# Performance work log

Hardware: AMD Instinct MI355X
Metric: run time of the kernel (lower is better)

The kernel has to match this reference:

```python
import jax, jax.numpy as jnp
import numpy as np

B, T, S, PD = 512, 2048, 16, 4

def setup_inputs() -> dict:
    key = jax.random.key(0)
    ks = jax.random.split(key, 10)
    w = lambda k, sh: (jax.random.normal(k, sh, dtype=jnp.float32) * 0.1)
    return {
        'z': jax.random.normal(ks[0], (B, T, S), dtype=jnp.float32),
        'p': jax.random.normal(ks[1], (B, T, PD), dtype=jnp.float32),
        'mu0': jnp.zeros((B, S), dtype=jnp.float32),
        'P0': jnp.full((B, S), 0.1, dtype=jnp.float32),  # cfg['kf_P0']
        'Wq1': w(ks[2], (PD, 64)), 'bq1': jnp.zeros((64,), jnp.float32),
        'Wq2': w(ks[3], (64, S)),  'bq2': jnp.zeros((S,), jnp.float32),
        'Wr1': w(ks[4], (PD, 64)), 'br1': jnp.zeros((64,), jnp.float32),
        'Wr2': w(ks[5], (64, S)),  'br2': jnp.zeros((S,), jnp.float32),
        'Wg1': w(ks[6], (PD, 32)), 'bg1': jnp.zeros((32,), jnp.float32),
        'Wg2': w(ks[7], (32, 1)),  'bg2': jnp.zeros((1,), jnp.float32),
    }

def _mlp(x, W1, b1, W2, b2):
    return jax.nn.relu(x @ W1 + b1) @ W2 + b2

def reference(z, p, mu0, P0, Wq1, bq1, Wq2, bq2, Wr1, br1, Wr2, br2, Wg1, bg1, Wg2, bg2):
    # z: [B,T,S], p: [B,T,PD]; scan over time with batched Kalman state.
    zT = jnp.swapaxes(z, 0, 1)  # [T,B,S]
    pT = jnp.swapaxes(p, 0, 1)  # [T,B,PD]

    def step(carry, inp):
        mu, P = carry            # [B,S], [B,S]
        z_t, p_t = inp           # [B,S], [B,PD]
        Q_t = jax.nn.softplus(_mlp(p_t, Wq1, bq1, Wq2, bq2)) + 1e-8
        R_t = jax.nn.softplus(_mlp(p_t, Wr1, br1, Wr2, br2)) + 1e-8
        P_pred = P + Q_t
        K = jnp.clip(P_pred / (P_pred + R_t), 1e-6, 0.95)
        gamma_t = jax.nn.sigmoid(_mlp(p_t, Wg1, bg1, Wg2, bg2))  # [B,1] (scalar per sample)
        mu_new = mu + gamma_t * (K * (z_t - mu))
        P_new = (1.0 - K) * P_pred
        return (mu_new, P_new), mu_new

    (mu_f, P_f), mus = jax.lax.scan(step, (mu0, P0), (zT, pT))
    return jnp.swapaxes(mus, 0, 1)  # [B,T,S]
```

## Files before the change

kernel.cpp:

```cpp
#include <hip/hip_runtime.h>
#include <hip/hip_fp16.h>
#include <stdint.h>
#include <math.h>

#define KB 512
#define KT 2048
#define KS 16
#define KPD 4

typedef _Float16 f16;
typedef _Float16 f16x4v __attribute__((ext_vector_type(4)));
typedef _Float16 f16x8 __attribute__((ext_vector_type(8)));
typedef float f32x4 __attribute__((ext_vector_type(4)));

#define MFMA16(A, B, C) __builtin_amdgcn_mfma_f32_16x16x32_f16(A, B, C, 0, 0, 0)

__device__ __forceinline__ float softplus_f(float x) {
    float ax = fabsf(x);
    float e  = __expf(-ax);
    return fmaxf(x, 0.0f) + __logf(1.0f + e);
}
__device__ __forceinline__ float sigmoid_f(float x) {
    return __builtin_amdgcn_rcpf(1.0f + __expf(-x));
}
__device__ __forceinline__ float h2f_lo(uint32_t w) {
    return __half2float(__ushort_as_half((unsigned short)(w & 0xffffu)));
}
__device__ __forceinline__ float h2f_hi(uint32_t w) {
    return __half2float(__ushort_as_half((unsigned short)(w >> 16)));
}
__device__ __forceinline__ f16x8 zero8() {
    f16x8 v;
#pragma unroll
    for (int i = 0; i < 8; ++i) v[i] = (f16)0;
    return v;
}

#define HRS 168

__global__ __launch_bounds__(64) void mlp_kernel(
    const float* __restrict__ p,
    const float* __restrict__ Wq1, const float* __restrict__ bq1,
    const float* __restrict__ Wq2, const float* __restrict__ bq2,
    const float* __restrict__ Wr1, const float* __restrict__ br1,
    const float* __restrict__ Wr2, const float* __restrict__ br2,
    const float* __restrict__ Wg1, const float* __restrict__ bg1,
    const float* __restrict__ Wg2, const float* __restrict__ bg2,
    uint32_t* __restrict__ qr_ws, float* __restrict__ g_ws)
{
    __shared__ __align__(16) f16 Hl[64][HRS];
    __shared__ __align__(16) f16 Pl[64][4];

    const int l = threadIdx.x;
    const int g = l >> 4;
    const int c = l & 15;
    const int row0 = blockIdx.x * 64;
    const int b = row0 >> 11;
    const int t0 = row0 & (KT - 1);

    f16x8 fA1[10];
#pragma unroll
    for (int m = 0; m < 10; ++m) {
        const float* W = (m < 4) ? (Wq1 + m * 16)
                       : (m < 8) ? (Wr1 + (m - 4) * 16)
                                 : (Wg1 + (m - 8) * 16);
        const int ld = (m < 8) ? 64 : 32;
        float w0 = W[0 * ld + c], w1 = W[1 * ld + c],
              w2 = W[2 * ld + c], w3 = W[3 * ld + c];
        f16x8 a = zero8();
        if (g == 0) { a[0] = (f16)w0; a[1] = (f16)w1; a[2] = (f16)w2; a[3] = (f16)w3; }
        fA1[m] = a;
    }

    f16x8 fA2[5];
#pragma unroll
    for (int i = 0; i < 4; ++i) {
        const float* W = (i < 2) ? Wq2 : Wr2;
        const int kb = (i & 1) * 32;
        f16x8 a;
#pragma unroll
        for (int j = 0; j < 8; ++j) a[j] = (f16)W[(kb + g * 8 + j) * 16 + c];
        fA2[i] = a;
    }
    {
        f16x8 a = zero8();
        if (c == 0) {
#pragma unroll
            for (int j = 0; j < 8; ++j) a[j] = (f16)Wg2[g * 8 + j];
        }
        fA2[4] = a;
    }

    const float bQ0 = bq2[g * 4 + 0], bQ1 = bq2[g * 4 + 1],
                bQ2 = bq2[g * 4 + 2], bQ3 = bq2[g * 4 + 3];
    const float bR0 = br2[g * 4 + 0], bR1 = br2[g * 4 + 1],
                bR2 = br2[g * 4 + 2], bR3 = br2[g * 4 + 3];
    const float bG = bg2[0];

    {
        const float4 pv = *reinterpret_cast<const float4*>(p + (size_t)(row0 + l) * KPD);
        f16x4v v; v[0] = (f16)pv.x; v[1] = (f16)pv.y; v[2] = (f16)pv.z; v[3] = (f16)pv.w;
        *reinterpret_cast<f16x4v*>(&Pl[l][0]) = v;
    }
    asm volatile("s_waitcnt lgkmcnt(0)" ::: "memory");
    __builtin_amdgcn_sched_barrier(0);

    f16x8 fBP[4];
#pragma unroll
    for (int n = 0; n < 4; ++n) {
        f16x8 v = zero8();
        if (g == 0) {
            f16x4v q = *reinterpret_cast<const f16x4v*>(&Pl[n * 16 + c][0]);
            v[0] = q[0]; v[1] = q[1]; v[2] = q[2]; v[3] = q[3];
        }
        fBP[n] = v;
    }

#pragma unroll
    for (int m = 0; m < 10; ++m) {
        const float* bs = (m < 4) ? (bq1 + m * 16)
                        : (m < 8) ? (br1 + (m - 4) * 16)
                                  : (bg1 + (m - 8) * 16);
        const float b0 = bs[g * 4 + 0], b1 = bs[g * 4 + 1],
                    b2 = bs[g * 4 + 2], b3 = bs[g * 4 + 3];
#pragma unroll
        for (int n = 0; n < 4; ++n) {
            f32x4 acc; acc[0] = b0; acc[1] = b1; acc[2] = b2; acc[3] = b3;
            acc = MFMA16(fA1[m], fBP[n], acc);
            auto h01 = __builtin_amdgcn_cvt_pkrtz(fmaxf(acc[0], 0.f), fmaxf(acc[1], 0.f));
            auto h23 = __builtin_amdgcn_cvt_pkrtz(fmaxf(acc[2], 0.f), fmaxf(acc[3], 0.f));
            uint2 w;
            __builtin_memcpy(&w.x, &h01, 4);
            __builtin_memcpy(&w.y, &h23, 4);
            *reinterpret_cast<uint2*>(&Hl[n * 16 + c][m * 16 + g * 4]) = w;
        }
    }
    asm volatile("s_waitcnt lgkmcnt(0)" ::: "memory");
    __builtin_amdgcn_sched_barrier(0);

#pragma unroll
    for (int n = 0; n < 4; ++n) {
        const int bt = n * 16 + c;
        f16x8 fb0 = *reinterpret_cast<const f16x8*>(&Hl[bt][0 * 32 + g * 8]);
        f16x8 fb1 = *reinterpret_cast<const f16x8*>(&Hl[bt][1 * 32 + g * 8]);
        f16x8 fb2 = *reinterpret_cast<const f16x8*>(&Hl[bt][2 * 32 + g * 8]);
        f16x8 fb3 = *reinterpret_cast<const f16x8*>(&Hl[bt][3 * 32 + g * 8]);
        f16x8 fb4 = *reinterpret_cast<const f16x8*>(&Hl[bt][4 * 32 + g * 8]);

        f32x4 aq; aq[0] = bQ0; aq[1] = bQ1; aq[2] = bQ2; aq[3] = bQ3;
        aq = MFMA16(fA2[0], fb0, aq);
        aq = MFMA16(fA2[1], fb1, aq);
        f32x4 ar; ar[0] = bR0; ar[1] = bR1; ar[2] = bR2; ar[3] = bR3;
        ar = MFMA16(fA2[2], fb2, ar);
        ar = MFMA16(fA2[3], fb3, ar);
        f32x4 ag; ag[0] = 0.f; ag[1] = 0.f; ag[2] = 0.f; ag[3] = 0.f;
        ag = MFMA16(fA2[4], fb4, ag);

        uint32_t* qdst = qr_ws + ((size_t)b * KS + g * 4) * KT + t0 + bt;
#pragma unroll
        for (int i = 0; i < 4; ++i) {
            float Qv = softplus_f(aq[i]) + 1e-8f;
            float Rv = softplus_f(ar[i]) + 1e-8f;
            auto pk = __builtin_amdgcn_cvt_pkrtz(Qv, Rv);
            uint32_t w; __builtin_memcpy(&w, &pk, 4);
            qdst[(size_t)i * KT] = w;
        }
        if (g == 0)
            g_ws[(size_t)b * KT + t0 + bt] = sigmoid_f(ag[0] + bG);
    }
}

#define QT 512
#define NQ (KT / QT)
#define CL 8

__global__ __launch_bounds__(1024) void scan_kernel(
    const uint32_t* __restrict__ qr_ws, const float* __restrict__ g_ws,
    const float* __restrict__ z, const float* __restrict__ mu0,
    const float* __restrict__ P0, float* __restrict__ out)
{
    __shared__ float smem[QT * 17 + QT];
    float* zmu = smem;
    float* gl  = smem + QT * 17;

    const int b = blockIdx.x;
    const int tid = threadIdx.x;
    const int lane = tid & 63;
    const int s = tid >> 6;

    const uint32_t* qrow = qr_ws + (size_t)(b * KS + s) * KT;
    const float* zb = z + (size_t)b * KT * KS;
    const float* gb = g_ws + (size_t)b * KT;
    float* ob = out + (size_t)b * KT * KS;

    float P_q  = P0[b * KS + s];
    float mu_q = mu0[b * KS + s];

    for (int q = 0; q < NQ; ++q) {
        const int t0 = q * QT;

        {
            const float4* zq = reinterpret_cast<const float4*>(zb + (size_t)t0 * KS);
#pragma unroll
            for (int v = 0; v < 2; ++v) {
                int k = tid * 2 + v;
                float4 w = zq[k];
                int t = k >> 2, s0 = (k & 3) << 2;
                zmu[t * 17 + s0 + 0] = w.x;
                zmu[t * 17 + s0 + 1] = w.y;
                zmu[t * 17 + s0 + 2] = w.z;
                zmu[t * 17 + s0 + 3] = w.w;
            }
            if (tid < QT) gl[tid] = gb[t0 + tid];
        }
        __syncthreads();

        uint32_t qr[CL];
        {
            const uint4* qp = reinterpret_cast<const uint4*>(qrow + t0 + lane * CL);
            uint4 u0 = qp[0], u1 = qp[1];
            qr[0] = u0.x; qr[1] = u0.y; qr[2] = u0.z; qr[3] = u0.w;
            qr[4] = u1.x; qr[5] = u1.y; qr[6] = u1.z; qr[7] = u1.w;
        }
        float c00 = 1.f, c01 = 0.f, c10 = 0.f, c11 = 1.f;
#pragma unroll
        for (int i = 0; i < CL; ++i) {
            float Q = h2f_lo(qr[i]), R = h2f_hi(qr[i]);
            float ta = fmaf(Q, c10, c00);
            float tb = fmaf(Q, c11, c01);
            float n10 = fmaf(Q + R, c10, c00);
            float n11 = fmaf(Q + R, c11, c01);
            c00 = R * ta; c01 = R * tb; c10 = n10; c11 = n11;
        }
        float rn = __builtin_amdgcn_rcpf(c11);
        float ma = c00 * rn, mb = c01 * rn, mc = c10 * rn;

#pragma unroll
        for (int r = 0; r < 6; ++r) {
            const int d = 1 << r;
            float pa = __shfl_up(ma, d);
            float pb = __shfl_up(mb, d);
            float pc = __shfl_up(mc, d);
            float na = fmaf(ma, pa, mb * pc);
            float nb = fmaf(ma, pb, mb);
            float nc = fmaf(mc, pa, pc);
            float nd = fmaf(mc, pb, 1.f);
            float rr = __builtin_amdgcn_rcpf(nd);
            bool act = (lane >= d);
            ma = act ? na * rr : ma;
            mb = act ? nb * rr : mb;
            mc = act ? nc * rr : mc;
        }
        float ea = __shfl_up(ma, 1);
        float eb = __shfl_up(mb, 1);
        float ec = __shfl_up(mc, 1);
        if (lane == 0) { ea = 1.f; eb = 0.f; ec = 0.f; }
        float P = fmaf(ea, P_q, eb) * __builtin_amdgcn_rcpf(fmaf(ec, P_q, 1.f));

        float av[CL], bw[CL];
        float A = 1.f, Bv = 0.f;
#pragma unroll
        for (int i = 0; i < CL; ++i) {
            float Q = h2f_lo(qr[i]), R = h2f_hi(qr[i]);
            float Pp = P + Q;
            float K0 = Pp * __builtin_amdgcn_rcpf(Pp + R);
            float Kk = __builtin_amdgcn_fmed3f(K0, 1e-6f, 0.95f);
            int t = lane * CL + i;
            float g = gl[t];
            float gk = g * Kk;
            float zv = zmu[t * 17 + s];
            av[i] = 1.f - gk;
            bw[i] = gk * zv;
            P = fmaf(-Kk, Pp, Pp);
            A = A * av[i];
            Bv = fmaf(av[i], Bv, bw[i]);
        }
        float P_end = __shfl(P, 63);

#pragma unroll
        for (int r = 0; r < 6; ++r) {
            const int d = 1 << r;
            float pA = __shfl_up(A, d);
            float pB = __shfl_up(Bv, d);
            float nA = A * pA;
            float nB = fmaf(A, pB, Bv);
            bool act = (lane >= d);
            A  = act ? nA : A;
            Bv = act ? nB : Bv;
        }
        float eA = __shfl_up(A, 1);
        float eB = __shfl_up(Bv, 1);
        if (lane == 0) { eA = 1.f; eB = 0.f; }
        float mu = fmaf(eA, mu_q, eB);

        __syncthreads();

#pragma unroll
        for (int i = 0; i < CL; ++i) {
            mu = fmaf(av[i], mu, bw[i]);
            zmu[(lane * CL + i) * 17 + s] = mu;
        }
        float mu_end = __shfl(mu, 63);
        __syncthreads();

#pragma unroll
        for (int v = 0; v < 2; ++v) {
            int k = tid * 2 + v;
            int t = k >> 2, s0 = (k & 3) << 2;
            float4 w;
            w.x = zmu[t * 17 + s0 + 0];
            w.y = zmu[t * 17 + s0 + 1];
            w.z = zmu[t * 17 + s0 + 2];
            w.w = zmu[t * 17 + s0 + 3];
            *reinterpret_cast<float4*>(ob + (size_t)(t0 + t) * KS + s0) = w;
        }
        P_q  = P_end;
        mu_q = mu_end;
        __syncthreads();
    }
}

#define KTT 128
#define KNT (KT / KTT)
#define SROW (KS + 1)

__device__ __forceinline__ void mlp16(const float4 pv,
    const float* __restrict__ W1, const float* __restrict__ b1,
    const float* __restrict__ W2, const float* __restrict__ b2,
    float* __restrict__ acc)
{
#pragma unroll
    for (int j = 0; j < KS; ++j) acc[j] = b2[j];
#pragma unroll 4
    for (int k = 0; k < 64; ++k) {
        float hk = b1[k];
        hk = fmaf(pv.x, W1[k],       hk);
        hk = fmaf(pv.y, W1[64 + k],  hk);
        hk = fmaf(pv.z, W1[128 + k], hk);
        hk = fmaf(pv.w, W1[192 + k], hk);
        hk = fmaxf(hk, 0.0f);
#pragma unroll
        for (int j = 0; j < KS; ++j) acc[j] = fmaf(hk, W2[k * KS + j], acc[j]);
    }
}

__global__ __launch_bounds__(320, 2) void kalman_fused(
    const float* __restrict__ z, const float* __restrict__ p,
    const float* __restrict__ mu0, const float* __restrict__ P0,
    const float* __restrict__ Wq1, const float* __restrict__ bq1,
    const float* __restrict__ Wq2, const float* __restrict__ bq2,
    const float* __restrict__ Wr1, const float* __restrict__ br1,
    const float* __restrict__ Wr2, const float* __restrict__ br2,
    const float* __restrict__ Wg1, const float* __restrict__ bg1,
    const float* __restrict__ Wg2, const float* __restrict__ bg2,
    float* __restrict__ out)
{
    __shared__ float sQ[2][KTT][SROW];
    __shared__ float sR[2][KTT][SROW];
    __shared__ float sZf[2][KTT][KS];
    __shared__ float sGf[2][KTT];

    const int b = blockIdx.x;
    const int tid = threadIdx.x;
    const float* __restrict__ zb = z + (size_t)b * KT * KS;
    const float* __restrict__ pb = p + (size_t)b * KT * KPD;
    float* __restrict__ outb = out + (size_t)b * KT * KS;

    const bool is_mlp = (tid < 256);

    auto do_mlp_tile = [&](int tile, int buf) {
        const int tt = tid & (KTT - 1);
        const int t = tile * KTT + tt;
        const float4 pv = *reinterpret_cast<const float4*>(pb + (size_t)t * KPD);
        float acc[KS];
        if (tid < KTT) {
            mlp16(pv, Wq1, bq1, Wq2, bq2, acc);
#pragma unroll
            for (int j = 0; j < KS; ++j)
                sQ[buf][tt][j] = softplus_f(acc[j]) + 1e-8f;
            float ag = bg2[0];
#pragma unroll 8
            for (int k = 0; k < 32; ++k) {
                float hk = bg1[k];
                hk = fmaf(pv.x, Wg1[k],      hk);
                hk = fmaf(pv.y, Wg1[32 + k], hk);
                hk = fmaf(pv.z, Wg1[64 + k], hk);
                hk = fmaf(pv.w, Wg1[96 + k], hk);
                hk = fmaxf(hk, 0.0f);
                ag = fmaf(hk, Wg2[k], ag);
            }
            sGf[buf][tt] = sigmoid_f(ag);
        } else {
            mlp16(pv, Wr1, br1, Wr2, br2, acc);
#pragma unroll
            for (int j = 0; j < KS; ++j)
                sR[buf][tt][j] = softplus_f(acc[j]) + 1e-8f;
        }
        const float4* __restrict__ zt =
            reinterpret_cast<const float4*>(zb + (size_t)tile * KTT * KS);
        float4* __restrict__ zd = reinterpret_cast<float4*>(&sZf[buf][0][0]);
        zd[tid] = zt[tid];
        zd[tid + 256] = zt[tid + 256];
    };

    float mu = 0.0f, Pv = 0.0f;
    if (!is_mlp) {
        const int lane = tid - 256;
        if (lane < KS) {
            mu = mu0[(size_t)b * KS + lane];
            Pv = P0[(size_t)b * KS + lane];
        }
    }

    if (is_mlp) do_mlp_tile(0, 0);
    __syncthreads();

    for (int k = 0; k < KNT; ++k) {
        const int cur = k & 1;
        if (is_mlp) {
            if (k + 1 < KNT) do_mlp_tile(k + 1, cur ^ 1);
        } else {
            const int lane = tid - 256;
            if (lane < KS) {
                const int s = lane;
                for (int tt = 0; tt < KTT; ++tt) {
                    const float Ppred = Pv + sQ[cur][tt][s];
                    float Kk = Ppred * __builtin_amdgcn_rcpf(Ppred + sR[cur][tt][s]);
                    Kk = __builtin_amdgcn_fmed3f(Kk, 1e-6f, 0.95f);
                    mu = fmaf(sGf[cur][tt] * Kk, sZf[cur][tt][s] - mu, mu);
                    Pv = fmaf(-Kk, Ppred, Ppred);
                    outb[(size_t)(k * KTT + tt) * KS + s] = mu;
                }
            }
        }
        __syncthreads();
    }
}

extern "C" void kernel_launch(void* const* d_in, const int* in_sizes, int n_in,
                              void* d_out, int out_size, void* d_ws, size_t ws_size,
                              hipStream_t stream) {
    const float* z   = (const float*)d_in[0];
    const float* p   = (const float*)d_in[1];
    const float* mu0 = (const float*)d_in[2];
    const float* P0  = (const float*)d_in[3];
    const float* Wq1 = (const float*)d_in[4];
    const float* bq1 = (const float*)d_in[5];
    const float* Wq2 = (const float*)d_in[6];
    const float* bq2 = (const float*)d_in[7];
    const float* Wr1 = (const float*)d_in[8];
    const float* br1 = (const float*)d_in[9];
    const float* Wr2 = (const float*)d_in[10];
    const float* br2 = (const float*)d_in[11];
    const float* Wg1 = (const float*)d_in[12];
    const float* bg1 = (const float*)d_in[13];
    const float* Wg2 = (const float*)d_in[14];
    const float* bg2 = (const float*)d_in[15];
    float* out = (float*)d_out;

    const size_t QR_BYTES = (size_t)KB * KS * KT * 4;
    const size_t G_BYTES  = (size_t)KB * KT * 4;

    if (ws_size >= QR_BYTES + G_BYTES) {
        uint32_t* qr_ws = (uint32_t*)d_ws;
        float* g_ws = (float*)((char*)d_ws + QR_BYTES);
        hipLaunchKernelGGL(mlp_kernel, dim3((KB * KT) / 64), dim3(64), 0, stream,
                           p, Wq1, bq1, Wq2, bq2, Wr1, br1, Wr2, br2,
                           Wg1, bg1, Wg2, bg2, qr_ws, g_ws);
        hipLaunchKernelGGL(scan_kernel, dim3(KB), dim3(1024), 0, stream,
                           qr_ws, g_ws, z, mu0, P0, out);
    } else {
        hipLaunchKernelGGL(kalman_fused, dim3(KB), dim3(320), 0, stream,
                           z, p, mu0, P0, Wq1, bq1, Wq2, bq2,
                           Wr1, br1, Wr2, br2, Wg1, bg1, Wg2, bg2, out);
    }
}
```

Measured before the change: 105.1 us.

## Make MLP kernel persistent over 8 tiles and shrink hidden LDS buffer

```diff
diff --git a/kernel.cpp b/kernel.cpp
--- a/kernel.cpp
+++ b/kernel.cpp
@@ -37,8 +37,9 @@
 }
 
 #define HRS 168
-
-__global__ __launch_bounds__(64) void mlp_kernel(
+#define NT  8
+
+__global__ __launch_bounds__(64, 4) void mlp_kernel(
     const float* __restrict__ p,
     const float* __restrict__ Wq1, const float* __restrict__ bq1,
     const float* __restrict__ Wq2, const float* __restrict__ bq2,
@@ -48,15 +49,12 @@
     const float* __restrict__ Wg2, const float* __restrict__ bg2,
     uint32_t* __restrict__ qr_ws, float* __restrict__ g_ws)
 {
-    __shared__ __align__(16) f16 Hl[64][HRS];
+    __shared__ __align__(16) f16 Hl[16][HRS];
     __shared__ __align__(16) f16 Pl[64][4];
 
     const int l = threadIdx.x;
     const int g = l >> 4;
     const int c = l & 15;
-    const int row0 = blockIdx.x * 64;
-    const int b = row0 >> 11;
-    const int t0 = row0 & (KT - 1);
 
     f16x8 fA1[10];
 #pragma unroll
@@ -97,76 +95,81 @@
                 bR2 = br2[g * 4 + 2], bR3 = br2[g * 4 + 3];
     const float bG = bg2[0];
 
-    {
-        const float4 pv = *reinterpret_cast<const float4*>(p + (size_t)(row0 + l) * KPD);
-        f16x4v v; v[0] = (f16)pv.x; v[1] = (f16)pv.y; v[2] = (f16)pv.z; v[3] = (f16)pv.w;
-        *reinterpret_cast<f16x4v*>(&Pl[l][0]) = v;
-    }
-    asm volatile("s_waitcnt lgkmcnt(0)" ::: "memory");
-    __builtin_amdgcn_sched_barrier(0);
-
-    f16x8 fBP[4];
-#pragma unroll
-    for (int n = 0; n < 4; ++n) {
-        f16x8 v = zero8();
-        if (g == 0) {
-            f16x4v q = *reinterpret_cast<const f16x4v*>(&Pl[n * 16 + c][0]);
-            v[0] = q[0]; v[1] = q[1]; v[2] = q[2]; v[3] = q[3];
-        }
-        fBP[n] = v;
-    }
-
+    float b1f[10][4];
 #pragma unroll
     for (int m = 0; m < 10; ++m) {
         const float* bs = (m < 4) ? (bq1 + m * 16)
                         : (m < 8) ? (br1 + (m - 4) * 16)
                                   : (bg1 + (m - 8) * 16);
-        const float b0 = bs[g * 4 + 0], b1 = bs[g * 4 + 1],
-                    b2 = bs[g * 4 + 2], b3 = bs[g * 4 + 3];
+#pragma unroll
+        for (int i = 0; i < 4; ++i) b1f[m][i] = bs[g * 4 + i];
+    }
+
+    for (int it = 0; it < NT; ++it) {
+        const int row0 = (blockIdx.x * NT + it) * 64;
+        const int b = row0 >> 11;
+        const int t0 = row0 & (KT - 1);
+
+        {
+            asm volatile("s_waitcnt lgkmcnt(0)" ::: "memory");
+            const float4 pv = *reinterpret_cast<const float4*>(p + (size_t)(row0 + l) * KPD);
+            f16x4v v; v[0] = (f16)pv.x; v[1] = (f16)pv.y; v[2] = (f16)pv.z; v[3] = (f16)pv.w;
+            *reinterpret_cast<f16x4v*>(&Pl[l][0]) = v;
+        }
+        asm volatile("s_waitcnt lgkmcnt(0)" ::: "memory");
+        __builtin_amdgcn_sched_barrier(0);
+
 #pragma unroll
         for (int n = 0; n < 4; ++n) {
-            f32x4 acc; acc[0] = b0; acc[1] = b1; acc[2] = b2; acc[3] = b3;
-            acc = MFMA16(fA1[m], fBP[n], acc);
-            auto h01 = __builtin_amdgcn_cvt_pkrtz(fmaxf(acc[0], 0.f), fmaxf(acc[1], 0.f));
-            auto h23 = __builtin_amdgcn_cvt_pkrtz(fmaxf(acc[2], 0.f), fmaxf(acc[3], 0.f));
-            uint2 w;
-            __builtin_memcpy(&w.x, &h01, 4);
-            __builtin_memcpy(&w.y, &h23, 4);
-            *reinterpret_cast<uint2*>(&Hl[n * 16 + c][m * 16 + g * 4]) = w;
-        }
-    }
-    asm volatile("s_waitcnt lgkmcnt(0)" ::: "memory");
-    __builtin_amdgcn_sched_barrier(0);
-
-#pragma unroll
-    for (int n = 0; n < 4; ++n) {
-        const int bt = n * 16 + c;
-        f16x8 fb0 = *reinterpret_cast<const f16x8*>(&Hl[bt][0 * 32 + g * 8]);
-        f16x8 fb1 = *reinterpret_cast<const f16x8*>(&Hl[bt][1 * 32 + g * 8]);
-        f16x8 fb2 = *reinterpret_cast<const f16x8*>(&Hl[bt][2 * 32 + g * 8]);
-        f16x8 fb3 = *reinterpret_cast<const f16x8*>(&Hl[bt][3 * 32 + g * 8]);
-        f16x8 fb4 = *reinterpret_cast<const f16x8*>(&Hl[bt][4 * 32 + g * 8]);
-
-        f32x4 aq; aq[0] = bQ0; aq[1] = bQ1; aq[2] = bQ2; aq[3] = bQ3;
-        aq = MFMA16(fA2[0], fb0, aq);
-        aq = MFMA16(fA2[1], fb1, aq);
-        f32x4 ar; ar[0] = bR0; ar[1] = bR1; ar[2] = bR2; ar[3] = bR3;
-        ar = MFMA16(fA2[2], fb2, ar);
-        ar = MFMA16(fA2[3], fb3, ar);
-        f32x4 ag; ag[0] = 0.f; ag[1] = 0.f; ag[2] = 0.f; ag[3] = 0.f;
-        ag = MFMA16(fA2[4], fb4, ag);
-
-        uint32_t* qdst = qr_ws + ((size_t)b * KS + g * 4) * KT + t0 + bt;
-#pragma unroll
-        for (int i = 0; i < 4; ++i) {
-            float Qv = softplus_f(aq[i]) + 1e-8f;
-            float Rv = softplus_f(ar[i]) + 1e-8f;
-            auto pk = __builtin_amdgcn_cvt_pkrtz(Qv, Rv);
-            uint32_t w; __builtin_memcpy(&w, &pk, 4);
-            qdst[(size_t)i * KT] = w;
-        }
-        if (g == 0)
-            g_ws[(size_t)b * KT + t0 + bt] = sigmoid_f(ag[0] + bG);
+            f16x8 fBP = zero8();
+            if (g == 0) {
+                f16x4v q = *reinterpret_cast<const f16x4v*>(&Pl[n * 16 + c][0]);
+                fBP[0] = q[0]; fBP[1] = q[1]; fBP[2] = q[2]; fBP[3] = q[3];
+            }
+
+#pragma unroll
+            for (int m = 0; m < 10; ++m) {
+                f32x4 acc;
+                acc[0] = b1f[m][0]; acc[1] = b1f[m][1];
+                acc[2] = b1f[m][2]; acc[3] = b1f[m][3];
+                acc = MFMA16(fA1[m], fBP, acc);
+                auto h01 = __builtin_amdgcn_cvt_pkrtz(fmaxf(acc[0], 0.f), fmaxf(acc[1], 0.f));
+                auto h23 = __builtin_amdgcn_cvt_pkrtz(fmaxf(acc[2], 0.f), fmaxf(acc[3], 0.f));
+                uint2 w;
+                __builtin_memcpy(&w.x, &h01, 4);
+                __builtin_memcpy(&w.y, &h23, 4);
+                *reinterpret_cast<uint2*>(&Hl[c][m * 16 + g * 4]) = w;
+            }
+            asm volatile("s_waitcnt lgkmcnt(0)" ::: "memory");
+            __builtin_amdgcn_sched_barrier(0);
+
+            f16x8 fb0 = *reinterpret_cast<const f16x8*>(&Hl[c][0 * 32 + g * 8]);
+            f16x8 fb1 = *reinterpret_cast<const f16x8*>(&Hl[c][1 * 32 + g * 8]);
+            f16x8 fb2 = *reinterpret_cast<const f16x8*>(&Hl[c][2 * 32 + g * 8]);
+            f16x8 fb3 = *reinterpret_cast<const f16x8*>(&Hl[c][3 * 32 + g * 8]);
+            f16x8 fb4 = *reinterpret_cast<const f16x8*>(&Hl[c][4 * 32 + g * 8]);
+
+            f32x4 aq; aq[0] = bQ0; aq[1] = bQ1; aq[2] = bQ2; aq[3] = bQ3;
+            aq = MFMA16(fA2[0], fb0, aq);
+            aq = MFMA16(fA2[1], fb1, aq);
+            f32x4 ar; ar[0] = bR0; ar[1] = bR1; ar[2] = bR2; ar[3] = bR3;
+            ar = MFMA16(fA2[2], fb2, ar);
+            ar = MFMA16(fA2[3], fb3, ar);
+            f32x4 ag; ag[0] = 0.f; ag[1] = 0.f; ag[2] = 0.f; ag[3] = 0.f;
+            ag = MFMA16(fA2[4], fb4, ag);
+
+            uint32_t* qdst = qr_ws + ((size_t)b * KS + g * 4) * KT + t0 + n * 16 + c;
+#pragma unroll
+            for (int i = 0; i < 4; ++i) {
+                float Qv = softplus_f(aq[i]) + 1e-8f;
+                float Rv = softplus_f(ar[i]) + 1e-8f;
+                auto pk = __builtin_amdgcn_cvt_pkrtz(Qv, Rv);
+                uint32_t w; __builtin_memcpy(&w, &pk, 4);
+                qdst[(size_t)i * KT] = w;
+            }
+            if (g == 0)
+                g_ws[(size_t)b * KT + t0 + n * 16 + c] = sigmoid_f(ag[0] + bG);
+        }
     }
 }
 
@@ -464,7 +467,7 @@
     if (ws_size >= QR_BYTES + G_BYTES) {
         uint32_t* qr_ws = (uint32_t*)d_ws;
         float* g_ws = (float*)((char*)d_ws + QR_BYTES);
-        hipLaunchKernelGGL(mlp_kernel, dim3((KB * KT) / 64), dim3(64), 0, stream,
+        hipLaunchKernelGGL(mlp_kernel, dim3((KB * KT) / (64 * NT)), dim3(64), 0, stream,
                            p, Wq1, bq1, Wq2, bq2, Wr1, br1, Wr2, br2,
                            Wg1, bg1, Wg2, bg2, qr_ws, g_ws);
         hipLaunchKernelGGL(scan_kernel, dim3(KB), dim3(1024), 0, stream,
```

Result: slower. 145.2 us (+38.2%).

## Software-pipeline MLP layer-1 and layer-2 GEMMs with double-buffered LDS tile

Applied to the files above, without the earlier changes.

```diff
diff --git a/kernel.cpp b/kernel.cpp
--- a/kernel.cpp
+++ b/kernel.cpp
@@ -48,7 +48,7 @@
     const float* __restrict__ Wg2, const float* __restrict__ bg2,
     uint32_t* __restrict__ qr_ws, float* __restrict__ g_ws)
 {
-    __shared__ __align__(16) f16 Hl[64][HRS];
+    __shared__ __align__(16) f16 Hl[2][16][HRS];
     __shared__ __align__(16) f16 Pl[64][4];
 
     const int l = threadIdx.x;
@@ -116,36 +116,31 @@
         fBP[n] = v;
     }
 
-#pragma unroll
-    for (int m = 0; m < 10; ++m) {
-        const float* bs = (m < 4) ? (bq1 + m * 16)
-                        : (m < 8) ? (br1 + (m - 4) * 16)
-                                  : (bg1 + (m - 8) * 16);
-        const float b0 = bs[g * 4 + 0], b1 = bs[g * 4 + 1],
-                    b2 = bs[g * 4 + 2], b3 = bs[g * 4 + 3];
-#pragma unroll
-        for (int n = 0; n < 4; ++n) {
-            f32x4 acc; acc[0] = b0; acc[1] = b1; acc[2] = b2; acc[3] = b3;
+    auto gemm1 = [&](int n, int buf) {
+#pragma unroll
+        for (int m = 0; m < 10; ++m) {
+            const float* bs = (m < 4) ? (bq1 + m * 16)
+                            : (m < 8) ? (br1 + (m - 4) * 16)
+                                      : (bg1 + (m - 8) * 16);
+            f32x4 acc;
+            acc[0] = bs[g * 4 + 0]; acc[1] = bs[g * 4 + 1];
+            acc[2] = bs[g * 4 + 2]; acc[3] = bs[g * 4 + 3];
             acc = MFMA16(fA1[m], fBP[n], acc);
             auto h01 = __builtin_amdgcn_cvt_pkrtz(fmaxf(acc[0], 0.f), fmaxf(acc[1], 0.f));
             auto h23 = __builtin_amdgcn_cvt_pkrtz(fmaxf(acc[2], 0.f), fmaxf(acc[3], 0.f));
             uint2 w;
             __builtin_memcpy(&w.x, &h01, 4);
             __builtin_memcpy(&w.y, &h23, 4);
-            *reinterpret_cast<uint2*>(&Hl[n * 16 + c][m * 16 + g * 4]) = w;
-        }
-    }
-    asm volatile("s_waitcnt lgkmcnt(0)" ::: "memory");
-    __builtin_amdgcn_sched_barrier(0);
-
-#pragma unroll
-    for (int n = 0; n < 4; ++n) {
-        const int bt = n * 16 + c;
-        f16x8 fb0 = *reinterpret_cast<const f16x8*>(&Hl[bt][0 * 32 + g * 8]);
-        f16x8 fb1 = *reinterpret_cast<const f16x8*>(&Hl[bt][1 * 32 + g * 8]);
-        f16x8 fb2 = *reinterpret_cast<const f16x8*>(&Hl[bt][2 * 32 + g * 8]);
-        f16x8 fb3 = *reinterpret_cast<const f16x8*>(&Hl[bt][3 * 32 + g * 8]);
-        f16x8 fb4 = *reinterpret_cast<const f16x8*>(&Hl[bt][4 * 32 + g * 8]);
+            *reinterpret_cast<uint2*>(&Hl[buf][c][m * 16 + g * 4]) = w;
+        }
+    };
+
+    auto gemm2 = [&](int n, int buf) {
+        f16x8 fb0 = *reinterpret_cast<const f16x8*>(&Hl[buf][c][0 * 32 + g * 8]);
+        f16x8 fb1 = *reinterpret_cast<const f16x8*>(&Hl[buf][c][1 * 32 + g * 8]);
+        f16x8 fb2 = *reinterpret_cast<const f16x8*>(&Hl[buf][c][2 * 32 + g * 8]);
+        f16x8 fb3 = *reinterpret_cast<const f16x8*>(&Hl[buf][c][3 * 32 + g * 8]);
+        f16x8 fb4 = *reinterpret_cast<const f16x8*>(&Hl[buf][c][4 * 32 + g * 8]);
 
         f32x4 aq; aq[0] = bQ0; aq[1] = bQ1; aq[2] = bQ2; aq[3] = bQ3;
         aq = MFMA16(fA2[0], fb0, aq);
@@ -156,7 +151,7 @@
         f32x4 ag; ag[0] = 0.f; ag[1] = 0.f; ag[2] = 0.f; ag[3] = 0.f;
         ag = MFMA16(fA2[4], fb4, ag);
 
-        uint32_t* qdst = qr_ws + ((size_t)b * KS + g * 4) * KT + t0 + bt;
+        uint32_t* qdst = qr_ws + ((size_t)b * KS + g * 4) * KT + t0 + n * 16 + c;
 #pragma unroll
         for (int i = 0; i < 4; ++i) {
             float Qv = softplus_f(aq[i]) + 1e-8f;
@@ -166,7 +161,14 @@
             qdst[(size_t)i * KT] = w;
         }
         if (g == 0)
-            g_ws[(size_t)b * KT + t0 + bt] = sigmoid_f(ag[0] + bG);
+            g_ws[(size_t)b * KT + t0 + n * 16 + c] = sigmoid_f(ag[0] + bG);
+    };
+
+    gemm1(0, 0);
+#pragma unroll
+    for (int n = 0; n < 4; ++n) {
+        if (n < 3) gemm1(n + 1, (n + 1) & 1);
+        gemm2(n, n & 1);
     }
 }
 
```

Measured after the change: 106.2 us. Within noise of the previous version (+1.1%).
